# Kernel optimization log

Hardware: AMD Instinct MI355X
Metric: run time of the kernel (lower is better)

## Reference

```python
import jax, jax.numpy as jnp
import numpy as np

N_NODES = 100000
N_EDGES = 3200000
IN_FEATS = 128
H_FEATS = 128
NUM_HEADS = 4
NEG_SLOPE = 0.2  # DGL GATConv default


def setup_inputs() -> dict:
    key = jax.random.key(0)
    ks = jax.random.split(key, 12)
    d = {}
    d["in_feat"] = jax.random.normal(ks[0], (N_NODES, IN_FEATS), jnp.float32)
    d["edge_weights"] = jax.random.uniform(ks[1], (N_EDGES,), jnp.float32)
    d["src"] = jax.random.randint(ks[2], (N_EDGES,), 0, N_NODES, jnp.int32)
    d["dst"] = jax.random.randint(ks[3], (N_EDGES,), 0, N_NODES, jnp.int32)
    s = 1.0 / np.sqrt(IN_FEATS)
    d["W0"] = jax.random.normal(ks[4], (IN_FEATS, H_FEATS), jnp.float32) * s
    d["attn_l0"] = jax.random.normal(ks[5], (NUM_HEADS, H_FEATS // NUM_HEADS), jnp.float32) * s
    d["attn_r0"] = jax.random.normal(ks[6], (NUM_HEADS, H_FEATS // NUM_HEADS), jnp.float32) * s
    d["bias0"] = jnp.zeros((H_FEATS,), jnp.float32)
    d["W1"] = jax.random.normal(ks[7], (H_FEATS, H_FEATS), jnp.float32) * s
    d["attn_l1"] = jax.random.normal(ks[8], (NUM_HEADS, H_FEATS // NUM_HEADS), jnp.float32) * s
    d["attn_r1"] = jax.random.normal(ks[9], (NUM_HEADS, H_FEATS // NUM_HEADS), jnp.float32) * s
    d["bias1"] = jnp.zeros((H_FEATS,), jnp.float32)
    return d


def gat_layer(h, src, dst, ew, W, al, ar, b, n_nodes):
    H, Dh = al.shape
    feat = (h @ W).reshape(n_nodes, H, Dh)          # [N,H,Dh]
    el = jnp.sum(feat * al[None], axis=-1)          # [N,H]
    er = jnp.sum(feat * ar[None], axis=-1)          # [N,H]
    e = jax.nn.leaky_relu(el[src] + er[dst], NEG_SLOPE)  # [E,H]
    # segment softmax over destination neighborhoods
    m = jax.ops.segment_max(e, dst, num_segments=n_nodes)
    m = jnp.where(jnp.isfinite(m), m, 0.0)
    ex = jnp.exp(e - m[dst])
    s = jax.ops.segment_sum(ex, dst, num_segments=n_nodes)
    a = ex / jnp.maximum(s[dst], 1e-20)             # [E,H]
    a = a * ew[:, None]                             # edge-weight scaling (post-softmax, as in DGL)
    msg = a[:, :, None] * feat[src]                 # [E,H,Dh]
    out = jax.ops.segment_sum(msg, dst, num_segments=n_nodes)
    out = out + b.reshape(1, H, Dh)
    return jax.nn.elu(out).reshape(n_nodes, H * Dh)


def reference(in_feat, edge_weights, src, dst, W0, attn_l0, attn_r0, bias0, W1, attn_l1, attn_r1, bias1):
    n = in_feat.shape[0]
    h = gat_layer(in_feat, src, dst, edge_weights, W0, attn_l0, attn_r0, bias0, n)
    h = gat_layer(h, src, dst, edge_weights, W1, attn_l1, attn_r1, bias1, n)
    return h
```

## Files before the change

kernel.cpp:

```cpp
#include <hip/hip_runtime.h>
#include <hip/hip_fp16.h>
#include <math.h>

#define NEG_SLOPE 0.2f
#define NPB 256
#define MAXB 512
#define A1_BS 1024

static __device__ __forceinline__ float leaky(float x) { return fmaxf(x, NEG_SLOPE * x); }

__global__ void k_zero(int* p, int n) {
    int i = blockIdx.x * blockDim.x + threadIdx.x;
    if (i < n) p[i] = 0;
}


__global__ __launch_bounds__(256) void k_bcount(const int* __restrict__ dst,
                                                int* __restrict__ bcnt, int n_edges, int nb) {
    __shared__ int h[MAXB];
    for (int i = threadIdx.x; i < nb; i += blockDim.x) h[i] = 0;
    __syncthreads();
    int stride = gridDim.x * blockDim.x;
    for (int e = blockIdx.x * blockDim.x + threadIdx.x; e < n_edges; e += stride)
        atomicAdd(&h[dst[e] >> 8], 1);
    __syncthreads();
    for (int i = threadIdx.x; i < nb; i += blockDim.x)
        if (h[i]) atomicAdd(&bcnt[i], h[i]);
}

__global__ __launch_bounds__(MAXB) void k_bscan(const int* __restrict__ bcnt,
                                                int* __restrict__ boffB,
                                                int* __restrict__ bcur, int nb) {
    __shared__ int s[MAXB];
    int t = threadIdx.x;
    int v = (t < nb) ? bcnt[t] : 0;
    s[t] = v;
    __syncthreads();
    for (int off = 1; off < MAXB; off <<= 1) {
        int x = (t >= off) ? s[t - off] : 0;
        __syncthreads();
        s[t] += x;
        __syncthreads();
    }
    if (t < nb) {
        int ex = s[t] - v;
        boffB[t] = ex;
        bcur[t] = ex;
    }
}

__global__ __launch_bounds__(A1_BS) void k_bin(const int* __restrict__ src,
                                               const int* __restrict__ dst,
                                               const float* __restrict__ ew,
                                               int* __restrict__ bcur,
                                               int2* __restrict__ recS,
                                               int n_edges, int chunk, int nb) {
    __shared__ int cnt[MAXB];
    __shared__ int base[MAXB];
    int t = threadIdx.x;
    int e0 = blockIdx.x * chunk;
    int e1 = e0 + chunk;
    if (e1 > n_edges) e1 = n_edges;
    for (int i = t; i < nb; i += A1_BS) cnt[i] = 0;
    __syncthreads();
    for (int e = e0 + t; e < e1; e += A1_BS) atomicAdd(&cnt[dst[e] >> 8], 1);
    __syncthreads();
    for (int i = t; i < nb; i += A1_BS) {
        int c = cnt[i];
        base[i] = c ? atomicAdd(&bcur[i], c) : 0;
        cnt[i] = 0;
    }
    __syncthreads();
    for (int e = e0 + t; e < e1; e += A1_BS) {
        int d = dst[e];
        int b = d >> 8;
        int p = base[b] + atomicAdd(&cnt[b], 1);
        recS[p] = make_int2(src[e] | ((d & (NPB - 1)) << 20), __float_as_int(ew[e]));
    }
}

__global__ __launch_bounds__(NPB) void k_buildcsr(const int* __restrict__ boffB,
                                                  const int* __restrict__ bcnt,
                                                  const int2* __restrict__ recS,
                                                  int* __restrict__ row_ptr,
                                                  int2* __restrict__ csr,
                                                  int n_nodes, int n_edges) {
    __shared__ int hist[NPB];
    __shared__ int pre[NPB];
    int b = blockIdx.x;
    int t = threadIdx.x;
    hist[t] = 0;
    __syncthreads();
    int off = boffB[b];
    int end = off + bcnt[b];
    for (int i = off + t; i < end; i += NPB)
        atomicAdd(&hist[(recS[i].x >> 20) & (NPB - 1)], 1);
    __syncthreads();
    int v = hist[t];
    pre[t] = v;
    __syncthreads();
    for (int o = 1; o < NPB; o <<= 1) {
        int x = (t >= o) ? pre[t - o] : 0;
        __syncthreads();
        pre[t] += x;
        __syncthreads();
    }
    int ex = pre[t] - v;
    int node = b * NPB + t;
    if (node < n_nodes) row_ptr[node] = off + ex;
    if (node == n_nodes - 1) row_ptr[n_nodes] = n_edges;
    if (b == 0 && t < 8) csr[n_edges + t] = make_int2(0, 0);
    hist[t] = off + ex;
    __syncthreads();
    for (int i = off + t; i < end; i += NPB) {
        int2 r = recS[i];
        int dl = (r.x >> 20) & (NPB - 1);
        int p = atomicAdd(&hist[dl], 1);
        csr[p] = make_int2(r.x & 0xFFFFF, r.y);
    }
}

__global__ __launch_bounds__(256) void k_gemm(const float* __restrict__ A,
                                              const float* __restrict__ B,
                                              __half* __restrict__ C,
                                              const float* __restrict__ al,
                                              const float* __restrict__ ar,
                                              float* __restrict__ el,
                                              float* __restrict__ er, int n) {
    __shared__ float Bs[128 * 64];
    int t = threadIdx.x;
    int row0 = blockIdx.x * 64;
    int colbase = blockIdx.y * 64;

    {
        int c0 = (t & 15) * 4;
        int kr = t >> 4;
        for (int it = 0; it < 8; ++it) {
            int k = kr + it * 16;
            float4 v = *(const float4*)(B + (size_t)k * 128 + colbase + c0);
            *(float4*)(Bs + k * 64 + c0) = v;
        }
    }
    __syncthreads();

    int r0 = row0 + (t >> 4) * 4;
    int c0 = (t & 15) * 4;
    const float* Ar0 = A + (size_t)((r0 + 0) < n ? (r0 + 0) : 0) * 128;
    const float* Ar1 = A + (size_t)((r0 + 1) < n ? (r0 + 1) : 0) * 128;
    const float* Ar2 = A + (size_t)((r0 + 2) < n ? (r0 + 2) : 0) * 128;
    const float* Ar3 = A + (size_t)((r0 + 3) < n ? (r0 + 3) : 0) * 128;

    float acc[4][4];
#pragma unroll
    for (int i = 0; i < 4; i++)
#pragma unroll
        for (int j = 0; j < 4; j++) acc[i][j] = 0.f;

#pragma unroll 2
    for (int k = 0; k < 128; k += 4) {
        float4 a0 = *(const float4*)(Ar0 + k);
        float4 a1 = *(const float4*)(Ar1 + k);
        float4 a2 = *(const float4*)(Ar2 + k);
        float4 a3 = *(const float4*)(Ar3 + k);
#pragma unroll
        for (int kk = 0; kk < 4; kk++) {
            float4 b = *(const float4*)(Bs + (k + kk) * 64 + c0);
            float e0 = kk == 0 ? a0.x : kk == 1 ? a0.y : kk == 2 ? a0.z : a0.w;
            float e1 = kk == 0 ? a1.x : kk == 1 ? a1.y : kk == 2 ? a1.z : a1.w;
            float e2 = kk == 0 ? a2.x : kk == 1 ? a2.y : kk == 2 ? a2.z : a2.w;
            float e3 = kk == 0 ? a3.x : kk == 1 ? a3.y : kk == 2 ? a3.z : a3.w;
            acc[0][0] = fmaf(e0, b.x, acc[0][0]); acc[0][1] = fmaf(e0, b.y, acc[0][1]);
            acc[0][2] = fmaf(e0, b.z, acc[0][2]); acc[0][3] = fmaf(e0, b.w, acc[0][3]);
            acc[1][0] = fmaf(e1, b.x, acc[1][0]); acc[1][1] = fmaf(e1, b.y, acc[1][1]);
            acc[1][2] = fmaf(e1, b.z, acc[1][2]); acc[1][3] = fmaf(e1, b.w, acc[1][3]);
            acc[2][0] = fmaf(e2, b.x, acc[2][0]); acc[2][1] = fmaf(e2, b.y, acc[2][1]);
            acc[2][2] = fmaf(e2, b.z, acc[2][2]); acc[2][3] = fmaf(e2, b.w, acc[2][3]);
            acc[3][0] = fmaf(e3, b.x, acc[3][0]); acc[3][1] = fmaf(e3, b.y, acc[3][1]);
            acc[3][2] = fmaf(e3, b.z, acc[3][2]); acc[3][3] = fmaf(e3, b.w, acc[3][3]);
        }
    }

#pragma unroll
    for (int i = 0; i < 4; i++) {
        int r = r0 + i;
        if (r < n) {
            __half2 h01 = __floats2half2_rn(acc[i][0], acc[i][1]);
            __half2 h23 = __floats2half2_rn(acc[i][2], acc[i][3]);
            union { __half2 h[2]; uint2 u; } cv;
            cv.h[0] = h01;
            cv.h[1] = h23;
            *(uint2*)(C + (size_t)r * 128 + colbase + c0) = cv.u;
        }
    }

    {
        int hg = blockIdx.y * 2 + ((t >> 3) & 1);
        float4 a4 = *(const float4*)(al + hg * 32 + (t & 7) * 4);
        float4 b4 = *(const float4*)(ar + hg * 32 + (t & 7) * 4);
        float pel[4], per[4];
#pragma unroll
        for (int i = 0; i < 4; i++) {
            pel[i] = acc[i][0] * a4.x + acc[i][1] * a4.y + acc[i][2] * a4.z + acc[i][3] * a4.w;
            per[i] = acc[i][0] * b4.x + acc[i][1] * b4.y + acc[i][2] * b4.z + acc[i][3] * b4.w;
        }
#pragma unroll
        for (int m = 1; m < 8; m <<= 1) {
#pragma unroll
            for (int i = 0; i < 4; i++) {
                pel[i] += __shfl_xor(pel[i], m);
                per[i] += __shfl_xor(per[i], m);
            }
        }
        if ((t & 7) == 0) {
#pragma unroll
            for (int i = 0; i < 4; i++) {
                int r = r0 + i;
                if (r < n) {
                    el[(size_t)r * 4 + hg] = pel[i];
                    er[(size_t)r * 4 + hg] = per[i];
                }
            }
        }
    }
}

__global__ __launch_bounds__(256) void k_edge(const int* __restrict__ row_ptr,
                                              const int2* __restrict__ csr,
                                              const __half* __restrict__ feat,
                                              const float* __restrict__ el,
                                              const float* __restrict__ er,
                                              const float* __restrict__ bias,
                                              float* __restrict__ out, int n) {
    int wv = threadIdx.x >> 6;
    int lane = threadIdx.x & 63;
    int sub = lane >> 5;
    int li = lane & 31;
    int h = li >> 3;
    int v = blockIdx.x * 8 + wv * 2 + sub;
    bool active = v < n;
    int vc = active ? v : n - 1;

    int start = row_ptr[vc];
    int end = active ? row_ptr[vc + 1] : start;
    float er_h = er[(size_t)vc * 4 + h];

    int myT = (end - start + 3) >> 2;
    int otherT = __shfl(myT, lane ^ 32);
    int maxT = myT > otherT ? myT : otherT;

    int last = end - 1;
    if (last < start) last = start;

    float4 acc = make_float4(0.f, 0.f, 0.f, 0.f);
    float ssum = 0.f;

    for (int j = 0; j < maxT; ++j) {
        int i = start + j * 4;
        int i0 = i < last ? i : last;
        int i1 = i + 1 < last ? i + 1 : last;
        int i2 = i + 2 < last ? i + 2 : last;
        int i3 = i + 3 < last ? i + 3 : last;
        float m0 = (i < end) ? 1.f : 0.f;
        float m1 = (i + 1 < end) ? 1.f : 0.f;
        float m2 = (i + 2 < end) ? 1.f : 0.f;
        float m3 = (i + 3 < end) ? 1.f : 0.f;
        int2 c0 = csr[i0];
        int2 c1 = csr[i1];
        int2 c2 = csr[i2];
        int2 c3 = csr[i3];
        float el0 = el[(size_t)c0.x * 4 + h];
        float el1 = el[(size_t)c1.x * 4 + h];
        float el2 = el[(size_t)c2.x * 4 + h];
        float el3 = el[(size_t)c3.x * 4 + h];
        uint2 r0 = ((const uint2*)(feat + (size_t)c0.x * 128))[li];
        uint2 r1 = ((const uint2*)(feat + (size_t)c1.x * 128))[li];
        uint2 r2 = ((const uint2*)(feat + (size_t)c2.x * 128))[li];
        uint2 r3 = ((const uint2*)(feat + (size_t)c3.x * 128))[li];
        float p0 = m0 * __expf(leaky(el0 + er_h));
        float p1 = m1 * __expf(leaky(el1 + er_h));
        float p2 = m2 * __expf(leaky(el2 + er_h));
        float p3 = m3 * __expf(leaky(el3 + er_h));
        ssum += (p0 + p1) + (p2 + p3);
        float w0 = p0 * __int_as_float(c0.y);
        float w1 = p1 * __int_as_float(c1.y);
        float w2 = p2 * __int_as_float(c2.y);
        float w3 = p3 * __int_as_float(c3.y);
        float2 a0 = __half22float2(*(__half2*)&r0.x);
        float2 b0 = __half22float2(*(__half2*)&r0.y);
        float2 a1 = __half22float2(*(__half2*)&r1.x);
        float2 b1 = __half22float2(*(__half2*)&r1.y);
        float2 a2 = __half22float2(*(__half2*)&r2.x);
        float2 b2 = __half22float2(*(__half2*)&r2.y);
        float2 a3 = __half22float2(*(__half2*)&r3.x);
        float2 b3 = __half22float2(*(__half2*)&r3.y);
        acc.x = fmaf(w0, a0.x, acc.x); acc.y = fmaf(w0, a0.y, acc.y);
        acc.z = fmaf(w0, b0.x, acc.z); acc.w = fmaf(w0, b0.y, acc.w);
        acc.x = fmaf(w1, a1.x, acc.x); acc.y = fmaf(w1, a1.y, acc.y);
        acc.z = fmaf(w1, b1.x, acc.z); acc.w = fmaf(w1, b1.y, acc.w);
        acc.x = fmaf(w2, a2.x, acc.x); acc.y = fmaf(w2, a2.y, acc.y);
        acc.z = fmaf(w2, b2.x, acc.z); acc.w = fmaf(w2, b2.y, acc.w);
        acc.x = fmaf(w3, a3.x, acc.x); acc.y = fmaf(w3, a3.y, acc.y);
        acc.z = fmaf(w3, b3.x, acc.z); acc.w = fmaf(w3, b3.y, acc.w);
    }

    if (active) {
        float inv = 1.f / fmaxf(ssum, 1e-20f);
        float4 bv = *(const float4*)(bias + li * 4);
        float o0 = fmaf(acc.x, inv, bv.x);
        float o1 = fmaf(acc.y, inv, bv.y);
        float o2 = fmaf(acc.z, inv, bv.z);
        float o3 = fmaf(acc.w, inv, bv.w);
        o0 = o0 > 0.f ? o0 : __expf(o0) - 1.f;
        o1 = o1 > 0.f ? o1 : __expf(o1) - 1.f;
        o2 = o2 > 0.f ? o2 : __expf(o2) - 1.f;
        o3 = o3 > 0.f ? o3 : __expf(o3) - 1.f;
        *(float4*)(out + (size_t)v * 128 + li * 4) = make_float4(o0, o1, o2, o3);
    }
}

extern "C" void kernel_launch(void* const* d_in, const int* in_sizes, int n_in,
                              void* d_out, int out_size, void* d_ws, size_t ws_size,
                              hipStream_t stream) {
    int n_nodes = in_sizes[0] / 128;
    int n_edges = in_sizes[1];

    const float* in_feat = (const float*)d_in[0];
    const float* ew = (const float*)d_in[1];
    const int* src = (const int*)d_in[2];
    const int* dst = (const int*)d_in[3];
    const float* W0 = (const float*)d_in[4];
    const float* al0 = (const float*)d_in[5];
    const float* ar0 = (const float*)d_in[6];
    const float* b0 = (const float*)d_in[7];
    const float* W1 = (const float*)d_in[8];
    const float* al1 = (const float*)d_in[9];
    const float* ar1 = (const float*)d_in[10];
    const float* b1 = (const float*)d_in[11];
    float* out = (float*)d_out;

    char* w = (char*)d_ws;
    auto alloc = [&](size_t bytes) {
        char* p = w;
        w += (bytes + 255) & ~(size_t)255;
        return p;
    };
    __half* featH = (__half*)alloc((size_t)n_nodes * 128 * 2);
    float* h1 = (float*)alloc((size_t)n_nodes * 128 * 4);
    float* el = (float*)alloc((size_t)n_nodes * 4 * 4);
    float* er = (float*)alloc((size_t)n_nodes * 4 * 4);
    int* row_ptr = (int*)alloc(((size_t)n_nodes + 1) * 4);
    int* bcnt = (int*)alloc(MAXB * 4);
    int* boffB = (int*)alloc(MAXB * 4);
    int* bcur = (int*)alloc(MAXB * 4);
    int2* csr = (int2*)alloc((size_t)n_edges * 8 + 64);

    int2* recS = (int2*)h1;

    int tb = 256;
    int nb2 = (n_nodes + NPB - 1) / NPB;

    k_zero<<<(MAXB + tb - 1) / tb, tb, 0, stream>>>(bcnt, nb2);
    k_bcount<<<256, tb, 0, stream>>>(dst, bcnt, n_edges, nb2);
    k_bscan<<<1, MAXB, 0, stream>>>(bcnt, boffB, bcur, nb2);
    int a1_grid = 256;
    int chunk = (n_edges + a1_grid - 1) / a1_grid;
    k_bin<<<a1_grid, A1_BS, 0, stream>>>(src, dst, ew, bcur, recS, n_edges, chunk, nb2);
    k_buildcsr<<<nb2, NPB, 0, stream>>>(boffB, bcnt, recS, row_ptr, csr, n_nodes, n_edges);

    dim3 gg((n_nodes + 63) / 64, 2);
    int ge = (n_nodes + 7) / 8;

    k_gemm<<<gg, 256, 0, stream>>>(in_feat, W0, featH, al0, ar0, el, er, n_nodes);
    k_edge<<<ge, 256, 0, stream>>>(row_ptr, csr, featH, el, er, b0, h1, n_nodes);

    k_gemm<<<gg, 256, 0, stream>>>(h1, W1, featH, al1, ar1, el, er, n_nodes);
    k_edge<<<ge, 256, 0, stream>>>(row_ptr, csr, featH, el, er, b1, out, n_nodes);
}
```

Measured before the change: 655.1 us.

## Sort edges by source block within each destination bucket when building CSR

The CSR build now stages each destination bucket in shared memory and counting-sorts it by source-node block before scattering into CSR order. Within each destination row the edges end up roughly ordered by source, which should improve locality of the feature gathers in the edge kernels. The cost is a second histogram and scan, a 512-thread block with about 80KB of shared memory (lower occupancy), and a fallback path for buckets larger than the buffer capacity.

```diff
diff --git a/kernel.cpp b/kernel.cpp
--- a/kernel.cpp
+++ b/kernel.cpp
@@ -6,6 +6,7 @@
 #define NPB 256
 #define MAXB 512
 #define A1_BS 1024
+#define BCAP 10240
 
 static __device__ __forceinline__ float leaky(float x) { return fmaxf(x, NEG_SLOPE * x); }
 
@@ -79,44 +80,82 @@
     }
 }
 
-__global__ __launch_bounds__(NPB) void k_buildcsr(const int* __restrict__ boffB,
-                                                  const int* __restrict__ bcnt,
-                                                  const int2* __restrict__ recS,
-                                                  int* __restrict__ row_ptr,
-                                                  int2* __restrict__ csr,
-                                                  int n_nodes, int n_edges) {
-    __shared__ int hist[NPB];
-    __shared__ int pre[NPB];
+__global__ __launch_bounds__(MAXB) void k_buildcsr(const int* __restrict__ boffB,
+                                                   const int* __restrict__ bcnt,
+                                                   const int2* __restrict__ recS,
+                                                   int* __restrict__ row_ptr,
+                                                   int2* __restrict__ csr,
+                                                   int n_nodes, int n_edges) {
+    __shared__ int2 buf[BCAP];
+    __shared__ int hsrc[MAXB];
+    __shared__ int tmp[MAXB];
+    __shared__ int hdst[NPB];
+    __shared__ int cdst[NPB];
     int b = blockIdx.x;
     int t = threadIdx.x;
-    hist[t] = 0;
+    for (int i = t; i < MAXB; i += MAXB) hsrc[i] = 0;
+    if (t < NPB) hdst[t] = 0;
     __syncthreads();
     int off = boffB[b];
-    int end = off + bcnt[b];
-    for (int i = off + t; i < end; i += NPB)
-        atomicAdd(&hist[(recS[i].x >> 20) & (NPB - 1)], 1);
-    __syncthreads();
-    int v = hist[t];
-    pre[t] = v;
+    int cnt = bcnt[b];
+    int end = off + cnt;
+
+    for (int i = off + t; i < end; i += MAXB) {
+        int x = recS[i].x;
+        atomicAdd(&hsrc[(x & 0xFFFFF) >> 8], 1);
+        atomicAdd(&hdst[(x >> 20) & (NPB - 1)], 1);
+    }
+    __syncthreads();
+
+    int vs = hsrc[t];
+    tmp[t] = vs;
+    __syncthreads();
+    for (int o = 1; o < MAXB; o <<= 1) {
+        int x = (t >= o) ? tmp[t - o] : 0;
+        __syncthreads();
+        tmp[t] += x;
+        __syncthreads();
+    }
+    hsrc[t] = tmp[t] - vs;
+    __syncthreads();
+
+    int vd = (t < NPB) ? hdst[t] : 0;
+    if (t < NPB) tmp[t] = vd;
     __syncthreads();
     for (int o = 1; o < NPB; o <<= 1) {
-        int x = (t >= o) ? pre[t - o] : 0;
-        __syncthreads();
-        pre[t] += x;
-        __syncthreads();
-    }
-    int ex = pre[t] - v;
-    int node = b * NPB + t;
-    if (node < n_nodes) row_ptr[node] = off + ex;
-    if (node == n_nodes - 1) row_ptr[n_nodes] = n_edges;
+        int x = (t >= o && t < NPB) ? tmp[t - o] : 0;
+        __syncthreads();
+        if (t < NPB) tmp[t] += x;
+        __syncthreads();
+    }
+    if (t < NPB) {
+        int ex = tmp[t] - vd;
+        int node = b * NPB + t;
+        if (node < n_nodes) row_ptr[node] = off + ex;
+        if (node == n_nodes - 1) row_ptr[n_nodes] = n_edges;
+        cdst[t] = off + ex;
+    }
     if (b == 0 && t < 8) csr[n_edges + t] = make_int2(0, 0);
-    hist[t] = off + ex;
-    __syncthreads();
-    for (int i = off + t; i < end; i += NPB) {
-        int2 r = recS[i];
-        int dl = (r.x >> 20) & (NPB - 1);
-        int p = atomicAdd(&hist[dl], 1);
-        csr[p] = make_int2(r.x & 0xFFFFF, r.y);
+    __syncthreads();
+
+    if (cnt <= BCAP) {
+        for (int i = off + t; i < end; i += MAXB) {
+            int2 r = recS[i];
+            int p = atomicAdd(&hsrc[(r.x & 0xFFFFF) >> 8], 1);
+            buf[p] = r;
+        }
+        __syncthreads();
+        for (int i = t; i < cnt; i += MAXB) {
+            int2 r = buf[i];
+            int p = atomicAdd(&cdst[(r.x >> 20) & (NPB - 1)], 1);
+            csr[p] = make_int2(r.x & 0xFFFFF, r.y);
+        }
+    } else {
+        for (int i = off + t; i < end; i += MAXB) {
+            int2 r = recS[i];
+            int p = atomicAdd(&cdst[(r.x >> 20) & (NPB - 1)], 1);
+            csr[p] = make_int2(r.x & 0xFFFFF, r.y);
+        }
     }
 }
 
@@ -365,7 +404,7 @@
     int a1_grid = 256;
     int chunk = (n_edges + a1_grid - 1) / a1_grid;
     k_bin<<<a1_grid, A1_BS, 0, stream>>>(src, dst, ew, bcur, recS, n_edges, chunk, nb2);
-    k_buildcsr<<<nb2, NPB, 0, stream>>>(boffB, bcnt, recS, row_ptr, csr, n_nodes, n_edges);
+    k_buildcsr<<<nb2, MAXB, 0, stream>>>(boffB, bcnt, recS, row_ptr, csr, n_nodes, n_edges);
 
     dim3 gg((n_nodes + 63) / 64, 2);
     int ge = (n_nodes + 7) / 8;
```

After: 658.2 us. About the same (+0.5%).
